# Kernel optimization log

Measured on AMD Instinct MI355X. Metric: run time of the kernel, lower is better.

The kernel has to match this reference:

```python
import jax, jax.numpy as jnp
import numpy as np

# model constants (match init_kwargs)
D_EQUI = 64
D_INV = 256
D_INV_COND = 256
D_MSG = 64
N_HEADS = 16
D_FF = 256
D_EDGE_IN = 64
D_EDGE_OUT = 64
D_OUT = D_EQUI + N_HEADS + D_EDGE_OUT  # 144
IN_FEATS = 2 * D_MSG + D_EQUI + D_EDGE_IN  # 256
NEG = -1e9

B, N, NC = 2, 256, 512


def setup_inputs() -> dict:
    key = jax.random.key(0)
    ks = jax.random.split(key, 20)
    s = 0.02
    inp = {
        'equis': jax.random.normal(ks[0], (B, N, 3, D_EQUI), jnp.float32),
        'invs': jax.random.normal(ks[1], (B, N, D_INV), jnp.float32),
        'cond_equis': jax.random.normal(ks[2], (B, NC, 3, D_EQUI), jnp.float32),
        'cond_invs': jax.random.normal(ks[3], (B, NC, D_INV_COND), jnp.float32),
        'edges': jax.random.normal(ks[4], (B, N, NC, D_EDGE_IN), jnp.float32),
        'adj_matrix': jax.random.randint(ks[5], (B, N, NC), 0, 2, jnp.int32),
        # pairwise message params
        'q_w': s * jax.random.normal(ks[6], (D_INV, D_MSG), jnp.float32),
        'q_b': jnp.zeros((D_MSG,), jnp.float32),
        'k_w': s * jax.random.normal(ks[7], (D_INV_COND, D_MSG), jnp.float32),
        'k_b': jnp.zeros((D_MSG,), jnp.float32),
        'w1': s * jax.random.normal(ks[8], (IN_FEATS, D_FF), jnp.float32),
        'b1': jnp.zeros((D_FF,), jnp.float32),
        'w2': s * jax.random.normal(ks[9], (D_FF, D_OUT), jnp.float32),
        'b2': jnp.zeros((D_OUT,), jnp.float32),
        # equi attention params (bias-free linears)
        'equi_in_w': s * jax.random.normal(ks[10], (D_EQUI, D_EQUI), jnp.float32),
        'equi_out_w': s * jax.random.normal(ks[11], (D_EQUI, D_EQUI), jnp.float32),
        # inv attention params
        'inv_in_w': s * jax.random.normal(ks[12], (D_INV_COND, D_INV_COND), jnp.float32),
        'inv_in_b': jnp.zeros((D_INV_COND,), jnp.float32),
        'inv_out_w': s * jax.random.normal(ks[13], (D_INV_COND, D_INV), jnp.float32),
        'inv_out_b': jnp.zeros((D_INV,), jnp.float32),
    }
    return inp


def reference(equis, invs, cond_equis, cond_invs, edges, adj_matrix,
              q_w, q_b, k_w, k_b, w1, b1, w2, b2,
              equi_in_w, equi_out_w, inv_in_w, inv_in_b, inv_out_w, inv_out_b):
    # adjacency -> additive attention mask [B,N,NC]
    mask = jnp.where(adj_matrix > 0, 0.0, NEG).astype(equis.dtype)

    # ---- pairwise messages ----
    # per-channel dot products over the coordinate axis: [B,N,NC,D_EQUI]
    dot = jnp.einsum('bqxd,bkxd->bqkd', equis, cond_equis)
    q_msg = invs @ q_w + q_b            # [B,N,D_MSG]
    k_msg = cond_invs @ k_w + k_b       # [B,NC,D_MSG]
    feats = jnp.concatenate([
        jnp.broadcast_to(q_msg[:, :, None, :], (B, N, NC, D_MSG)),
        jnp.broadcast_to(k_msg[:, None, :, :], (B, N, NC, D_MSG)),
        dot,
        edges,
    ], axis=-1)                          # [B,N,NC,IN_FEATS]
    h = jax.nn.silu(feats @ w1 + b1)
    messages = h @ w2 + b2               # [B,N,NC,D_OUT]

    equi_m = messages[..., :D_EQUI]
    inv_m = messages[..., D_EQUI:D_EQUI + N_HEADS]
    edge_out = messages[..., D_EQUI + N_HEADS:]

    # ---- equivariant attention ----
    proj = jnp.einsum('bkxd,de->bkxe', cond_equis, equi_in_w)  # [B,NC,3,D_EQUI]
    attn_e = jax.nn.softmax(equi_m + mask[..., None], axis=2)   # [B,N,NC,D_EQUI]
    eo = jnp.einsum('bqkd,bkxd->bqxd', attn_e, proj)            # [B,N,3,D_EQUI]
    w_e = jnp.sqrt(jnp.sum(attn_e ** 2, axis=2))                # [B,N,D_EQUI]
    eo = eo * w_e[:, :, None, :]
    equi_out = jnp.einsum('bqxd,de->bqxe', eo, equi_out_w)

    # ---- invariant attention ----
    pf = cond_invs @ inv_in_w + inv_in_b                        # [B,NC,D_INV_COND]
    hf = pf.reshape(B, NC, N_HEADS, D_INV_COND // N_HEADS)      # [B,NC,H,dh]
    attn_i = jax.nn.softmax(inv_m + mask[..., None], axis=2)    # [B,N,NC,H]
    io = jnp.einsum('bqkh,bkhd->bqhd', attn_i, hf)              # [B,N,H,dh]
    w_i = jnp.sqrt(jnp.sum(attn_i ** 2, axis=2))                # [B,N,H]
    io = (io * w_i[..., None]).reshape(B, N, D_INV_COND)
    inv_out = io @ inv_out_w + inv_out_b                        # [B,N,D_INV]

    return equi_out, inv_out, edge_out
```

## Files before the change

### kernel.cpp

```cpp
#include <hip/hip_runtime.h>
#include <hip/hip_bf16.h>

#define DEVINL static __device__ __forceinline__

typedef __attribute__((ext_vector_type(8))) short bf16x8;
typedef __attribute__((ext_vector_type(8))) unsigned short us8;
typedef __attribute__((ext_vector_type(4))) float f32x4;
typedef __attribute__((ext_vector_type(4))) unsigned short us4;

DEVINL float siluf(float x) { return x / (1.0f + __expf(-x)); }
DEVINL unsigned short bfb(float x) { __hip_bfloat16 h = __float2bfloat16(x); return *(unsigned short*)&h; }
DEVINL float b2f(unsigned short u) { return __uint_as_float(((unsigned int)u) << 16); }

__global__ __launch_bounds__(256) void prep_all(
    const float* __restrict__ invs, const float* __restrict__ cond_invs,
    const float* __restrict__ cond_equis,
    const float* __restrict__ q_w, const float* __restrict__ q_b,
    const float* __restrict__ k_w, const float* __restrict__ k_b,
    const float* __restrict__ w1, const float* __restrict__ b1,
    const float* __restrict__ w2,
    const float* __restrict__ equi_in_w,
    const float* __restrict__ inv_in_w, const float* __restrict__ inv_in_b,
    unsigned short* __restrict__ w1f, unsigned short* __restrict__ w2f,
    float* __restrict__ km, float* __restrict__ hq,
    float* __restrict__ projt, float* __restrict__ pft) {
  __shared__ float smem_f[1024];
  const int blk = blockIdx.x, tid = threadIdx.x;

  if (blk < 25) {
    const int g = blk;
    if (g < 16) {
      #pragma unroll
      for (int e2 = 0; e2 < 16; ++e2) {
        const int flat = tid * 16 + e2;
        const int kk = flat >> 9, rem = flat & 511, ln = rem >> 3, e = rem & 7;
        const int c = g * 16 + (ln & 15);
        const int k = kk * 32 + (ln >> 4) * 8 + e;
        w1f[(size_t)g * 4096 + flat] = bfb(w1[(size_t)k * 256 + c]);
      }
    } else {
      const int t = g - 16;
      #pragma unroll
      for (int e2 = 0; e2 < 16; ++e2) {
        const int flat = tid * 16 + e2;
        const int kk = flat >> 9, rem = flat & 511, ln = rem >> 3, e = rem & 7;
        const int c = t * 16 + (ln & 15);
        const int k = kk * 32 + (ln >> 4) * 8 + e;
        w2f[(size_t)t * 4096 + flat] = bfb(w2[(size_t)k * 144 + c]);
      }
    }
    return;
  }
  if (blk < 281) {
    const int row = (blk - 25) * 4 + (tid >> 6), c = tid & 63;
    float* srow = smem_f + (tid >> 6) * 256;
    for (int k = c; k < 256; k += 64) srow[k] = cond_invs[(size_t)row * 256 + k];
    __syncthreads();
    float a = k_b[c];
    for (int k = 0; k < 256; ++k) a += srow[k] * k_w[(size_t)k * 64 + c];
    km[(size_t)row * 64 + c] = a;
    return;
  }
  if (blk < 1049) {
    const int r = (blk - 281) * 4 + (tid >> 6), c = tid & 63;
    float* srow = smem_f + (tid >> 6) * 64;
    srow[c] = cond_equis[(size_t)r * 64 + c];
    __syncthreads();
    float a = 0.f;
    for (int k = 0; k < 64; ++k) a += srow[k] * equi_in_w[(size_t)k * 64 + c];
    const int b = r / 1536, rr = r % 1536, kn = rr / 3, x = rr % 3;
    projt[((size_t)(b * 3 + x) * 64 + c) * 512 + kn] = a;
    return;
  }
  if (blk < 2073) {
    const int r = blk - 1049, b = r >> 9, kn = r & 511;
    smem_f[tid] = cond_invs[(size_t)r * 256 + tid];
    __syncthreads();
    float a = inv_in_b[tid];
    for (int k = 0; k < 256; ++k) a += smem_f[k] * inv_in_w[(size_t)k * 256 + tid];
    pft[((size_t)(b * 256) + tid) * 512 + kn] = a;
    return;
  }
  {
    const int r = blk - 2073;
    smem_f[tid] = invs[(size_t)r * 256 + tid];
    __syncthreads();
    if (tid < 64) {
      float a = q_b[tid];
      for (int k = 0; k < 256; ++k) a += smem_f[k] * q_w[(size_t)k * 64 + tid];
      smem_f[256 + tid] = a;
    }
    __syncthreads();
    float a = b1[tid];
    for (int d = 0; d < 64; ++d) a += smem_f[256 + d] * w1[(size_t)d * 256 + tid];
    hq[(size_t)r * 256 + tid] = a;
  }
}

__global__ __launch_bounds__(256, 2) void msg_kernel(
    const float* __restrict__ equis, const float* __restrict__ cond_equis,
    const float* __restrict__ edges,
    const float* __restrict__ hq, const float* __restrict__ km,
    const unsigned short* __restrict__ w1f,
    const unsigned short* __restrict__ w2f, const float* __restrict__ b2,
    float* __restrict__ edge_out, __hip_bfloat16* __restrict__ sct) {
  __shared__ __align__(16) unsigned short buf[64][264];
  unsigned short (*score_s)[92] = (unsigned short (*)[92])&buf[0][0];
  float (*edge_s)[68]           = (float (*)[68])((char*)&buf[0][0] + 11776);

  const int bq = blockIdx.x >> 3;
  const int b  = bq >> 8;
  const int k0 = (blockIdx.x & 7) * 64;
  const int tid = threadIdx.x;
  const int lane = tid & 63, wn = tid >> 6;
  const int lj  = lane & 15;
  const int lkb = (lane >> 4) * 8;
  const int lr4 = (lane >> 4) * 4;

  #pragma unroll
  for (int it = 0; it < 4; ++it) {
    const int flat = it * 256 + tid, row = flat >> 4, seg = flat & 15;
    const float4 v = *(const float4*)&km[((size_t)(b * 512 + k0 + row)) * 64 + seg * 4];
    us4 u = { bfb(v.x), bfb(v.y), bfb(v.z), bfb(v.w) };
    *(us4*)&buf[row][seg * 4] = u;
  }
  #pragma unroll
  for (int it = 0; it < 4; ++it) {
    const int flat = it * 256 + tid, row = flat >> 4, seg = flat & 15;
    const float4 v = *(const float4*)&edges[((size_t)bq * 512 + k0 + row) * 64 + seg * 4];
    us4 u = { bfb(v.x), bfb(v.y), bfb(v.z), bfb(v.w) };
    *(us4*)&buf[row][128 + seg * 4] = u;
  }
  {
    const int r = tid >> 2, dseg = tid & 3;
    const float* cer = cond_equis + ((size_t)(b * 512 + k0 + r)) * 192 + dseg * 16;
    const float* eqr = equis + (size_t)bq * 192 + dseg * 16;
    float dv[16];
    #pragma unroll
    for (int j = 0; j < 16; ++j) dv[j] = 0.f;
    #pragma unroll
    for (int sec = 0; sec < 3; ++sec) {
      #pragma unroll
      for (int q4 = 0; q4 < 4; ++q4) {
        const float4 cv = *(const float4*)&cer[sec * 64 + q4 * 4];
        const float4 ev = *(const float4*)&eqr[sec * 64 + q4 * 4];
        dv[q4 * 4 + 0] += cv.x * ev.x;
        dv[q4 * 4 + 1] += cv.y * ev.y;
        dv[q4 * 4 + 2] += cv.z * ev.z;
        dv[q4 * 4 + 3] += cv.w * ev.w;
      }
    }
    us8 o0, o1;
    #pragma unroll
    for (int j = 0; j < 8; ++j) { o0[j] = bfb(dv[j]); o1[j] = bfb(dv[8 + j]); }
    *(us8*)&buf[r][64 + dseg * 16] = o0;
    *(us8*)&buf[r][64 + dseg * 16 + 8] = o1;
  }
  __syncthreads();

#define LW1(BUF, KK) { \
    _Pragma("unroll") for (int ct = 0; ct < 4; ++ct) \
      BUF[ct] = *(const bf16x8*)&w1f[((size_t)(((wn * 4 + ct) * 8 + ((KK) + 2)) * 64) + lane) * 8]; }

#define G1STEP(KK, CUR, NXT, DOPF) { \
    if (DOPF) { LW1(NXT, (KK) + 1); } \
    bf16x8 fbv[4]; \
    _Pragma("unroll") for (int rt = 0; rt < 4; ++rt) \
      fbv[rt] = *(const bf16x8*)&buf[rt * 16 + lj][(KK) * 32 + lkb]; \
    _Pragma("unroll") for (int ct = 0; ct < 4; ++ct) \
      _Pragma("unroll") for (int rt = 0; rt < 4; ++rt) \
        acc[ct][rt] = __builtin_amdgcn_mfma_f32_16x16x32_bf16(CUR[ct], fbv[rt], acc[ct][rt], 0, 0, 0); }

#define LW2(BUF, KK) { \
    _Pragma("unroll") for (int it = 0; it < 3; ++it) { \
      const int t = it * 4 + wn; \
      if (t < 9) BUF[it] = *(const bf16x8*)&w2f[((size_t)((t * 8 + (KK)) * 64) + lane) * 8]; } }

#define G2STEP(KK, CUR, NXT, DOPF) { \
    if (DOPF) { LW2(NXT, (KK) + 1); } \
    bf16x8 fbv[4]; \
    _Pragma("unroll") for (int rt = 0; rt < 4; ++rt) \
      fbv[rt] = *(const bf16x8*)&buf[rt * 16 + lj][(KK) * 32 + lkb]; \
    _Pragma("unroll") for (int it = 0; it < 3; ++it) { \
      const int t = it * 4 + wn; \
      if (t < 9) { \
        _Pragma("unroll") for (int rt = 0; rt < 4; ++rt) \
          a2[it][rt] = __builtin_amdgcn_mfma_f32_16x16x32_bf16(CUR[it], fbv[rt], a2[it][rt], 0, 0, 0); \
      } } }

  f32x4 acc[4][4];
  #pragma unroll
  for (int ct = 0; ct < 4; ++ct) {
    const float4 hv = *(const float4*)&hq[(size_t)bq * 256 + wn * 64 + ct * 16 + lr4];
    #pragma unroll
    for (int rt = 0; rt < 4; ++rt) { acc[ct][rt][0] = hv.x; acc[ct][rt][1] = hv.y; acc[ct][rt][2] = hv.z; acc[ct][rt][3] = hv.w; }
  }
  {
    bf16x8 waA[4], waB[4];
    LW1(waA, 0);
    G1STEP(0, waA, waB, 1)
    G1STEP(1, waB, waA, 1)
    G1STEP(2, waA, waB, 1)
    G1STEP(3, waB, waA, 1)
    G1STEP(4, waA, waB, 1)
    G1STEP(5, waB, waA, 0)
  }
  __syncthreads();

  #pragma unroll
  for (int ct = 0; ct < 4; ++ct)
    #pragma unroll
    for (int rt = 0; rt < 4; ++rt) {
      us4 u = { bfb(siluf(acc[ct][rt][0])), bfb(siluf(acc[ct][rt][1])),
                bfb(siluf(acc[ct][rt][2])), bfb(siluf(acc[ct][rt][3])) };
      *(us4*)&buf[rt * 16 + lj][wn * 64 + ct * 16 + lr4] = u;
    }
  __syncthreads();

  f32x4 a2[3][4];
  #pragma unroll
  for (int it = 0; it < 3; ++it) {
    const int t = it * 4 + wn;
    if (t < 9) {
      const float4 bb = *(const float4*)&b2[t * 16 + lr4];
      #pragma unroll
      for (int rt = 0; rt < 4; ++rt) { a2[it][rt][0] = bb.x; a2[it][rt][1] = bb.y; a2[it][rt][2] = bb.z; a2[it][rt][3] = bb.w; }
    }
  }
  {
    bf16x8 wbA[3], wbB[3];
    LW2(wbA, 0);
    G2STEP(0, wbA, wbB, 1)
    G2STEP(1, wbB, wbA, 1)
    G2STEP(2, wbA, wbB, 1)
    G2STEP(3, wbB, wbA, 1)
    G2STEP(4, wbA, wbB, 1)
    G2STEP(5, wbB, wbA, 1)
    G2STEP(6, wbA, wbB, 1)
    G2STEP(7, wbB, wbA, 0)
  }
  __syncthreads();

  #pragma unroll
  for (int it = 0; it < 3; ++it) {
    const int t = it * 4 + wn;
    if (t < 9) {
      if (t < 5) {
        #pragma unroll
        for (int rt = 0; rt < 4; ++rt) {
          us4 u = { bfb(a2[it][rt][0]), bfb(a2[it][rt][1]), bfb(a2[it][rt][2]), bfb(a2[it][rt][3]) };
          *(us4*)&score_s[rt * 16 + lj][t * 16 + lr4] = u;
        }
      } else {
        #pragma unroll
        for (int rt = 0; rt < 4; ++rt) {
          float4 v; v.x = a2[it][rt][0]; v.y = a2[it][rt][1]; v.z = a2[it][rt][2]; v.w = a2[it][rt][3];
          *(float4*)&edge_s[rt * 16 + lj][(t - 5) * 16 + lr4] = v;
        }
      }
    }
  }
  __syncthreads();

  #pragma unroll
  for (int it = 0; it < 3; ++it) {
    const int idx = it * 256 + tid;
    if (idx < 640) {
      const int c = idx >> 3, s = idx & 7;
      bf16x8 v;
      #pragma unroll
      for (int j = 0; j < 8; ++j) v[j] = (short)score_s[s * 8 + j][c];
      *(bf16x8*)&sct[((size_t)bq * 80 + c) * 512 + k0 + s * 8] = v;
    }
  }
  #pragma unroll
  for (int it = 0; it < 4; ++it) {
    const int idx = it * 256 + tid;
    const int row = idx >> 4, sg = idx & 15;
    *(float4*)&edge_out[((size_t)bq * 512 + k0 + row) * 64 + sg * 4] = *(const float4*)&edge_s[row][sg * 4];
  }
#undef LW1
#undef G1STEP
#undef LW2
#undef G2STEP
}

__global__ __launch_bounds__(512) void attn_kernel(
    const __hip_bfloat16* __restrict__ sct, const int* __restrict__ adj,
    const float* __restrict__ projt, const float* __restrict__ pft,
    const float* __restrict__ eow, const float* __restrict__ iow,
    const float* __restrict__ iob, float* __restrict__ out) {
  __shared__ float eo_s[3][64];
  __shared__ float io_s[256];
  __shared__ __align__(16) float wred[8][64][20];

  const int bq = blockIdx.x, b = bq >> 8;
  const int tid = threadIdx.x, lane = tid & 63, w = tid >> 6;
  const int kb = lane * 8;

  const int4 aj0 = *(const int4*)&adj[(size_t)bq * 512 + kb];
  const int4 aj1 = *(const int4*)&adj[(size_t)bq * 512 + kb + 4];
  const unsigned int mk = (aj0.x > 0 ? 1u : 0) | (aj0.y > 0 ? 2u : 0) | (aj0.z > 0 ? 4u : 0) | (aj0.w > 0 ? 8u : 0)
                        | (aj1.x > 0 ? 16u : 0) | (aj1.y > 0 ? 32u : 0) | (aj1.z > 0 ? 64u : 0) | (aj1.w > 0 ? 128u : 0);

  for (int dd = 0; dd < 8; ++dd) {
    const int d = w * 8 + dd;
    const bf16x8 s8 = *(const bf16x8*)&sct[((size_t)bq * 80 + d) * 512 + kb];
    float p[8], z = 0.f, s2 = 0.f;
    #pragma unroll
    for (int j = 0; j < 8; ++j) {
      const float e = ((mk >> j) & 1) ? __expf(b2f((unsigned short)s8[j])) : 0.f;
      p[j] = e; z += e; s2 += e * e;
    }
    float ax[3];
    #pragma unroll
    for (int x = 0; x < 3; ++x) {
      const float* pr = projt + ((size_t)(b * 3 + x) * 64 + d) * 512 + kb;
      const float4 w0 = *(const float4*)pr;
      const float4 w1v = *(const float4*)(pr + 4);
      ax[x] = p[0] * w0.x + p[1] * w0.y + p[2] * w0.z + p[3] * w0.w
            + p[4] * w1v.x + p[5] * w1v.y + p[6] * w1v.z + p[7] * w1v.w;
    }
    #pragma unroll
    for (int off = 32; off; off >>= 1) {
      z += __shfl_xor(z, off, 64); s2 += __shfl_xor(s2, off, 64);
      ax[0] += __shfl_xor(ax[0], off, 64); ax[1] += __shfl_xor(ax[1], off, 64); ax[2] += __shfl_xor(ax[2], off, 64);
    }
    if (lane == 0) {
      const float sc = sqrtf(s2) / (z * z);
      eo_s[0][d] = ax[0] * sc; eo_s[1][d] = ax[1] * sc; eo_s[2][d] = ax[2] * sc;
    }
  }

  #pragma unroll
  for (int hh = 0; hh < 2; ++hh) {
    const int h = w * 2 + hh;
    const bf16x8 s8 = *(const bf16x8*)&sct[((size_t)bq * 80 + 64 + h) * 512 + kb];
    float p[8], z = 0.f, s2 = 0.f;
    #pragma unroll
    for (int j = 0; j < 8; ++j) {
      const float e = ((mk >> j) & 1) ? __expf(b2f((unsigned short)s8[j])) : 0.f;
      p[j] = e; z += e; s2 += e * e;
    }
    f32x4 io[4];
    #pragma unroll
    for (int d4 = 0; d4 < 4; ++d4)
      #pragma unroll
      for (int di = 0; di < 4; ++di) {
        const float* pr = pft + ((size_t)(b * 256) + h * 16 + d4 * 4 + di) * 512 + kb;
        const float4 w0 = *(const float4*)pr;
        const float4 w1v = *(const float4*)(pr + 4);
        io[d4][di] = p[0] * w0.x + p[1] * w0.y + p[2] * w0.z + p[3] * w0.w
                   + p[4] * w1v.x + p[5] * w1v.y + p[6] * w1v.z + p[7] * w1v.w;
      }
    #pragma unroll
    for (int off = 32; off; off >>= 1) { z += __shfl_xor(z, off, 64); s2 += __shfl_xor(s2, off, 64); }
    #pragma unroll
    for (int d4 = 0; d4 < 4; ++d4) {
      float4 vv; vv.x = io[d4][0]; vv.y = io[d4][1]; vv.z = io[d4][2]; vv.w = io[d4][3];
      *(float4*)&wred[w][lane][d4 * 4] = vv;
    }
    const int g = lane >> 4, dd2 = lane & 15;
    float s = 0.f;
    #pragma unroll
    for (int j = 0; j < 16; ++j) s += wred[w][g * 16 + j][dd2];
    s += __shfl_xor(s, 16, 64);
    s += __shfl_xor(s, 32, 64);
    if (lane < 16) {
      const float sc = sqrtf(s2) / (z * z);
      io_s[h * 16 + dd2] = s * sc;
    }
  }
  __syncthreads();

  if (tid < 192) {
    const int x = tid >> 6, e = tid & 63;
    float a = 0.f;
    for (int d = 0; d < 64; ++d) a += eo_s[x][d] * eow[(size_t)d * 64 + e];
    out[(size_t)bq * 192 + x * 64 + e] = a;
  }
  if (tid < 256) {
    float a = iob[tid];
    for (int k = 0; k < 256; ++k) a += io_s[k] * iow[(size_t)k * 256 + tid];
    out[98304 + (size_t)bq * 256 + tid] = a;
  }
}

extern "C" void kernel_launch(void* const* d_in, const int* in_sizes, int n_in,
                              void* d_out, int out_size, void* d_ws, size_t ws_size,
                              hipStream_t stream) {
  const float* equis      = (const float*)d_in[0];
  const float* invs       = (const float*)d_in[1];
  const float* cond_equis = (const float*)d_in[2];
  const float* cond_invs  = (const float*)d_in[3];
  const float* edges      = (const float*)d_in[4];
  const int*   adj        = (const int*)d_in[5];
  const float* q_w  = (const float*)d_in[6];
  const float* q_b  = (const float*)d_in[7];
  const float* k_w  = (const float*)d_in[8];
  const float* k_b  = (const float*)d_in[9];
  const float* w1   = (const float*)d_in[10];
  const float* b1   = (const float*)d_in[11];
  const float* w2   = (const float*)d_in[12];
  const float* b2   = (const float*)d_in[13];
  const float* equi_in_w  = (const float*)d_in[14];
  const float* equi_out_w = (const float*)d_in[15];
  const float* inv_in_w   = (const float*)d_in[16];
  const float* inv_in_b   = (const float*)d_in[17];
  const float* inv_out_w  = (const float*)d_in[18];
  const float* inv_out_b  = (const float*)d_in[19];

  float* out = (float*)d_out;
  float* ws  = (float*)d_ws;
  unsigned short* w1f = (unsigned short*)ws;
  unsigned short* w2f = w1f + 65536;
  float* km    = ws + 51200;
  float* hq    = km + 65536;
  float* projt = hq + 131072;
  float* pft   = projt + 196608;
  __hip_bfloat16* sct = (__hip_bfloat16*)(pft + 262144);

  prep_all<<<2585, 256, 0, stream>>>(invs, cond_invs, cond_equis,
                                     q_w, q_b, k_w, k_b, w1, b1, w2,
                                     equi_in_w, inv_in_w, inv_in_b,
                                     w1f, w2f, km, hq, projt, pft);

  msg_kernel<<<4096, 256, 0, stream>>>(equis, cond_equis, edges, hq, km,
                                       w1f, w2f, b2,
                                       out + 229376 , sct);

  attn_kernel<<<512, 512, 0, stream>>>(sct, adj, projt, pft,
                                       equi_out_w, inv_out_w, inv_out_b, out);
}
```

Baseline: 156.5 us.

## Make msg_kernel persistent over four key tiles with software-prefetched inputs

Each msg_kernel block now handles four consecutive 64-key tiles (half of the keys for one query) instead of one, cutting the grid from 4096 to 1024 blocks. The next tile's km, edges and cond_equis values are loaded into registers before the first GEMM and written to a separate feats shared buffer during the hidden-activation phase, so global loads overlap MFMA work. Query equis are cached once in shared memory. The costs are more registers (prefetch buffers plus accumulators), more shared memory (a feats buffer in addition to hbuf), and fewer blocks, which may lower occupancy and load balance across CUs.

After: 397.8 us. +154.3%, slower.

```diff
diff --git a/kernel.cpp b/kernel.cpp
--- a/kernel.cpp
+++ b/kernel.cpp
@@ -104,59 +104,66 @@
     const unsigned short* __restrict__ w1f,
     const unsigned short* __restrict__ w2f, const float* __restrict__ b2,
     float* __restrict__ edge_out, __hip_bfloat16* __restrict__ sct) {
-  __shared__ __align__(16) unsigned short buf[64][264];
-  unsigned short (*score_s)[92] = (unsigned short (*)[92])&buf[0][0];
-  float (*edge_s)[68]           = (float (*)[68])((char*)&buf[0][0] + 11776);
-
-  const int bq = blockIdx.x >> 3;
+  __shared__ __align__(16) unsigned short feats[64][200];
+  __shared__ __align__(16) unsigned short hbuf[64][264];
+  __shared__ float eq_s[192];
+  unsigned short (*score_s)[92] = (unsigned short (*)[92])&hbuf[0][0];
+  float (*edge_s)[68]           = (float (*)[68])((char*)&hbuf[0][0] + 11776);
+
+  const int bq = blockIdx.x >> 1;
   const int b  = bq >> 8;
-  const int k0 = (blockIdx.x & 7) * 64;
+  const int kh = blockIdx.x & 1;
   const int tid = threadIdx.x;
   const int lane = tid & 63, wn = tid >> 6;
   const int lj  = lane & 15;
   const int lkb = (lane >> 4) * 8;
   const int lr4 = (lane >> 4) * 4;
 
-  #pragma unroll
-  for (int it = 0; it < 4; ++it) {
-    const int flat = it * 256 + tid, row = flat >> 4, seg = flat & 15;
-    const float4 v = *(const float4*)&km[((size_t)(b * 512 + k0 + row)) * 64 + seg * 4];
-    us4 u = { bfb(v.x), bfb(v.y), bfb(v.z), bfb(v.w) };
-    *(us4*)&buf[row][seg * 4] = u;
-  }
-  #pragma unroll
-  for (int it = 0; it < 4; ++it) {
-    const int flat = it * 256 + tid, row = flat >> 4, seg = flat & 15;
-    const float4 v = *(const float4*)&edges[((size_t)bq * 512 + k0 + row) * 64 + seg * 4];
-    us4 u = { bfb(v.x), bfb(v.y), bfb(v.z), bfb(v.w) };
-    *(us4*)&buf[row][128 + seg * 4] = u;
-  }
+  if (tid < 192) eq_s[tid] = equis[(size_t)bq * 192 + tid];
+
   {
-    const int r = tid >> 2, dseg = tid & 3;
-    const float* cer = cond_equis + ((size_t)(b * 512 + k0 + r)) * 192 + dseg * 16;
-    const float* eqr = equis + (size_t)bq * 192 + dseg * 16;
-    float dv[16];
-    #pragma unroll
-    for (int j = 0; j < 16; ++j) dv[j] = 0.f;
-    #pragma unroll
-    for (int sec = 0; sec < 3; ++sec) {
-      #pragma unroll
-      for (int q4 = 0; q4 < 4; ++q4) {
-        const float4 cv = *(const float4*)&cer[sec * 64 + q4 * 4];
-        const float4 ev = *(const float4*)&eqr[sec * 64 + q4 * 4];
-        dv[q4 * 4 + 0] += cv.x * ev.x;
-        dv[q4 * 4 + 1] += cv.y * ev.y;
-        dv[q4 * 4 + 2] += cv.z * ev.z;
-        dv[q4 * 4 + 3] += cv.w * ev.w;
-      }
-    }
-    us8 o0, o1;
-    #pragma unroll
-    for (int j = 0; j < 8; ++j) { o0[j] = bfb(dv[j]); o1[j] = bfb(dv[8 + j]); }
-    *(us8*)&buf[r][64 + dseg * 16] = o0;
-    *(us8*)&buf[r][64 + dseg * 16 + 8] = o1;
-  }
-  __syncthreads();
+    const int k0 = kh * 256;
+    #pragma unroll
+    for (int it = 0; it < 4; ++it) {
+      const int flat = it * 256 + tid, row = flat >> 4, seg = flat & 15;
+      const float4 v = *(const float4*)&km[((size_t)(b * 512 + k0 + row)) * 64 + seg * 4];
+      us4 u = { bfb(v.x), bfb(v.y), bfb(v.z), bfb(v.w) };
+      *(us4*)&feats[row][seg * 4] = u;
+    }
+    #pragma unroll
+    for (int it = 0; it < 4; ++it) {
+      const int flat = it * 256 + tid, row = flat >> 4, seg = flat & 15;
+      const float4 v = *(const float4*)&edges[((size_t)bq * 512 + k0 + row) * 64 + seg * 4];
+      us4 u = { bfb(v.x), bfb(v.y), bfb(v.z), bfb(v.w) };
+      *(us4*)&feats[row][128 + seg * 4] = u;
+    }
+    __syncthreads();
+    {
+      const int r = tid >> 2, dseg = tid & 3;
+      const float* cer = cond_equis + ((size_t)(b * 512 + k0 + r)) * 192 + dseg * 16;
+      float dv[16];
+      #pragma unroll
+      for (int j = 0; j < 16; ++j) dv[j] = 0.f;
+      #pragma unroll
+      for (int sec = 0; sec < 3; ++sec) {
+        #pragma unroll
+        for (int q4 = 0; q4 < 4; ++q4) {
+          const float4 cv = *(const float4*)&cer[sec * 64 + q4 * 4];
+          const float4 ev = *(const float4*)&eq_s[sec * 64 + dseg * 16 + q4 * 4];
+          dv[q4 * 4 + 0] += cv.x * ev.x;
+          dv[q4 * 4 + 1] += cv.y * ev.y;
+          dv[q4 * 4 + 2] += cv.z * ev.z;
+          dv[q4 * 4 + 3] += cv.w * ev.w;
+        }
+      }
+      us8 o0, o1;
+      #pragma unroll
+      for (int j = 0; j < 8; ++j) { o0[j] = bfb(dv[j]); o1[j] = bfb(dv[8 + j]); }
+      *(us8*)&feats[r][64 + dseg * 16] = o0;
+      *(us8*)&feats[r][64 + dseg * 16 + 8] = o1;
+    }
+    __syncthreads();
+  }
 
 #define LW1(BUF, KK) { \
     _Pragma("unroll") for (int ct = 0; ct < 4; ++ct) \
@@ -166,7 +173,7 @@
     if (DOPF) { LW1(NXT, (KK) + 1); } \
     bf16x8 fbv[4]; \
     _Pragma("unroll") for (int rt = 0; rt < 4; ++rt) \
-      fbv[rt] = *(const bf16x8*)&buf[rt * 16 + lj][(KK) * 32 + lkb]; \
+      fbv[rt] = *(const bf16x8*)&feats[rt * 16 + lj][(KK) * 32 + lkb]; \
     _Pragma("unroll") for (int ct = 0; ct < 4; ++ct) \
       _Pragma("unroll") for (int rt = 0; rt < 4; ++rt) \
         acc[ct][rt] = __builtin_amdgcn_mfma_f32_16x16x32_bf16(CUR[ct], fbv[rt], acc[ct][rt], 0, 0, 0); }
@@ -180,7 +187,7 @@
     if (DOPF) { LW2(NXT, (KK) + 1); } \
     bf16x8 fbv[4]; \
     _Pragma("unroll") for (int rt = 0; rt < 4; ++rt) \
-      fbv[rt] = *(const bf16x8*)&buf[rt * 16 + lj][(KK) * 32 + lkb]; \
+      fbv[rt] = *(const bf16x8*)&hbuf[rt * 16 + lj][(KK) * 32 + lkb]; \
     _Pragma("unroll") for (int it = 0; it < 3; ++it) { \
       const int t = it * 4 + wn; \
       if (t < 9) { \
@@ -188,96 +195,150 @@
           a2[it][rt] = __builtin_amdgcn_mfma_f32_16x16x32_bf16(CUR[it], fbv[rt], a2[it][rt], 0, 0, 0); \
       } } }
 
-  f32x4 acc[4][4];
-  #pragma unroll
-  for (int ct = 0; ct < 4; ++ct) {
-    const float4 hv = *(const float4*)&hq[(size_t)bq * 256 + wn * 64 + ct * 16 + lr4];
-    #pragma unroll
-    for (int rt = 0; rt < 4; ++rt) { acc[ct][rt][0] = hv.x; acc[ct][rt][1] = hv.y; acc[ct][rt][2] = hv.z; acc[ct][rt][3] = hv.w; }
-  }
-  {
-    bf16x8 waA[4], waB[4];
-    LW1(waA, 0);
-    G1STEP(0, waA, waB, 1)
-    G1STEP(1, waB, waA, 1)
-    G1STEP(2, waA, waB, 1)
-    G1STEP(3, waB, waA, 1)
-    G1STEP(4, waA, waB, 1)
-    G1STEP(5, waB, waA, 0)
-  }
-  __syncthreads();
-
-  #pragma unroll
-  for (int ct = 0; ct < 4; ++ct)
-    #pragma unroll
-    for (int rt = 0; rt < 4; ++rt) {
-      us4 u = { bfb(siluf(acc[ct][rt][0])), bfb(siluf(acc[ct][rt][1])),
-                bfb(siluf(acc[ct][rt][2])), bfb(siluf(acc[ct][rt][3])) };
-      *(us4*)&buf[rt * 16 + lj][wn * 64 + ct * 16 + lr4] = u;
-    }
-  __syncthreads();
-
-  f32x4 a2[3][4];
-  #pragma unroll
-  for (int it = 0; it < 3; ++it) {
-    const int t = it * 4 + wn;
-    if (t < 9) {
-      const float4 bb = *(const float4*)&b2[t * 16 + lr4];
-      #pragma unroll
-      for (int rt = 0; rt < 4; ++rt) { a2[it][rt][0] = bb.x; a2[it][rt][1] = bb.y; a2[it][rt][2] = bb.z; a2[it][rt][3] = bb.w; }
-    }
-  }
-  {
-    bf16x8 wbA[3], wbB[3];
-    LW2(wbA, 0);
-    G2STEP(0, wbA, wbB, 1)
-    G2STEP(1, wbB, wbA, 1)
-    G2STEP(2, wbA, wbB, 1)
-    G2STEP(3, wbB, wbA, 1)
-    G2STEP(4, wbA, wbB, 1)
-    G2STEP(5, wbB, wbA, 1)
-    G2STEP(6, wbA, wbB, 1)
-    G2STEP(7, wbB, wbA, 0)
-  }
-  __syncthreads();
-
-  #pragma unroll
-  for (int it = 0; it < 3; ++it) {
-    const int t = it * 4 + wn;
-    if (t < 9) {
-      if (t < 5) {
+  for (int t = 0; t < 4; ++t) {
+    const int k0  = kh * 256 + t * 64;
+    const int k0n = k0 + 64;
+    const bool pf = (t < 3);
+
+    float4 pkm[4], ped[4], pc[3][4];
+    if (pf) {
+      #pragma unroll
+      for (int it = 0; it < 4; ++it) {
+        const int flat = it * 256 + tid, row = flat >> 4, seg = flat & 15;
+        pkm[it] = *(const float4*)&km[((size_t)(b * 512 + k0n + row)) * 64 + seg * 4];
+        ped[it] = *(const float4*)&edges[((size_t)bq * 512 + k0n + row) * 64 + seg * 4];
+      }
+      const int r = tid >> 2, dseg = tid & 3;
+      const float* cer = cond_equis + ((size_t)(b * 512 + k0n + r)) * 192 + dseg * 16;
+      #pragma unroll
+      for (int sec = 0; sec < 3; ++sec)
         #pragma unroll
-        for (int rt = 0; rt < 4; ++rt) {
-          us4 u = { bfb(a2[it][rt][0]), bfb(a2[it][rt][1]), bfb(a2[it][rt][2]), bfb(a2[it][rt][3]) };
-          *(us4*)&score_s[rt * 16 + lj][t * 16 + lr4] = u;
+        for (int q4 = 0; q4 < 4; ++q4)
+          pc[sec][q4] = *(const float4*)&cer[sec * 64 + q4 * 4];
+    }
+
+    f32x4 acc[4][4];
+    #pragma unroll
+    for (int ct = 0; ct < 4; ++ct) {
+      const float4 hv = *(const float4*)&hq[(size_t)bq * 256 + wn * 64 + ct * 16 + lr4];
+      #pragma unroll
+      for (int rt = 0; rt < 4; ++rt) { acc[ct][rt][0] = hv.x; acc[ct][rt][1] = hv.y; acc[ct][rt][2] = hv.z; acc[ct][rt][3] = hv.w; }
+    }
+    {
+      bf16x8 waA[4], waB[4];
+      LW1(waA, 0);
+      G1STEP(0, waA, waB, 1)
+      G1STEP(1, waB, waA, 1)
+      G1STEP(2, waA, waB, 1)
+      G1STEP(3, waB, waA, 1)
+      G1STEP(4, waA, waB, 1)
+      G1STEP(5, waB, waA, 0)
+    }
+    __syncthreads();
+
+    #pragma unroll
+    for (int ct = 0; ct < 4; ++ct)
+      #pragma unroll
+      for (int rt = 0; rt < 4; ++rt) {
+        us4 u = { bfb(siluf(acc[ct][rt][0])), bfb(siluf(acc[ct][rt][1])),
+                  bfb(siluf(acc[ct][rt][2])), bfb(siluf(acc[ct][rt][3])) };
+        *(us4*)&hbuf[rt * 16 + lj][wn * 64 + ct * 16 + lr4] = u;
+      }
+    if (pf) {
+      #pragma unroll
+      for (int it = 0; it < 4; ++it) {
+        const int flat = it * 256 + tid, row = flat >> 4, seg = flat & 15;
+        us4 uk = { bfb(pkm[it].x), bfb(pkm[it].y), bfb(pkm[it].z), bfb(pkm[it].w) };
+        *(us4*)&feats[row][seg * 4] = uk;
+        us4 ue = { bfb(ped[it].x), bfb(ped[it].y), bfb(ped[it].z), bfb(ped[it].w) };
+        *(us4*)&feats[row][128 + seg * 4] = ue;
+      }
+      const int r = tid >> 2, dseg = tid & 3;
+      float dv[16];
+      #pragma unroll
+      for (int j = 0; j < 16; ++j) dv[j] = 0.f;
+      #pragma unroll
+      for (int sec = 0; sec < 3; ++sec) {
+        #pragma unroll
+        for (int q4 = 0; q4 < 4; ++q4) {
+          const float4 cv = pc[sec][q4];
+          const float4 ev = *(const float4*)&eq_s[sec * 64 + dseg * 16 + q4 * 4];
+          dv[q4 * 4 + 0] += cv.x * ev.x;
+          dv[q4 * 4 + 1] += cv.y * ev.y;
+          dv[q4 * 4 + 2] += cv.z * ev.z;
+          dv[q4 * 4 + 3] += cv.w * ev.w;
         }
-      } else {
+      }
+      us8 o0, o1;
+      #pragma unroll
+      for (int j = 0; j < 8; ++j) { o0[j] = bfb(dv[j]); o1[j] = bfb(dv[8 + j]); }
+      *(us8*)&feats[r][64 + dseg * 16] = o0;
+      *(us8*)&feats[r][64 + dseg * 16 + 8] = o1;
+    }
+    __syncthreads();
+
+    f32x4 a2[3][4];
+    #pragma unroll
+    for (int it = 0; it < 3; ++it) {
+      const int t2 = it * 4 + wn;
+      if (t2 < 9) {
+        const float4 bb = *(const float4*)&b2[t2 * 16 + lr4];
         #pragma unroll
-        for (int rt = 0; rt < 4; ++rt) {
-          float4 v; v.x = a2[it][rt][0]; v.y = a2[it][rt][1]; v.z = a2[it][rt][2]; v.w = a2[it][rt][3];
-          *(float4*)&edge_s[rt * 16 + lj][(t - 5) * 16 + lr4] = v;
+        for (int rt = 0; rt < 4; ++rt) { a2[it][rt][0] = bb.x; a2[it][rt][1] = bb.y; a2[it][rt][2] = bb.z; a2[it][rt][3] = bb.w; }
+      }
+    }
+    {
+      bf16x8 wbA[3], wbB[3];
+      LW2(wbA, 0);
+      G2STEP(0, wbA, wbB, 1)
+      G2STEP(1, wbB, wbA, 1)
+      G2STEP(2, wbA, wbB, 1)
+      G2STEP(3, wbB, wbA, 1)
+      G2STEP(4, wbA, wbB, 1)
+      G2STEP(5, wbB, wbA, 1)
+      G2STEP(6, wbA, wbB, 1)
+      G2STEP(7, wbB, wbA, 0)
+    }
+    __syncthreads();
+
+    #pragma unroll
+    for (int it = 0; it < 3; ++it) {
+      const int t2 = it * 4 + wn;
+      if (t2 < 9) {
+        if (t2 < 5) {
+          #pragma unroll
+          for (int rt = 0; rt < 4; ++rt) {
+            us4 u = { bfb(a2[it][rt][0]), bfb(a2[it][rt][1]), bfb(a2[it][rt][2]), bfb(a2[it][rt][3]) };
+            *(us4*)&score_s[rt * 16 + lj][t2 * 16 + lr4] = u;
+          }
+        } else {
+          #pragma unroll
+          for (int rt = 0; rt < 4; ++rt) {
+            float4 v; v.x = a2[it][rt][0]; v.y = a2[it][rt][1]; v.z = a2[it][rt][2]; v.w = a2[it][rt][3];
+            *(float4*)&edge_s[rt * 16 + lj][(t2 - 5) * 16 + lr4] = v;
+          }
         }
       }
     }
-  }
-  __syncthreads();
-
-  #pragma unroll
-  for (int it = 0; it < 3; ++it) {
-    const int idx = it * 256 + tid;
-    if (idx < 640) {
-      const int c = idx >> 3, s = idx & 7;
-      bf16x8 v;
-      #pragma unroll
-      for (int j = 0; j < 8; ++j) v[j] = (short)score_s[s * 8 + j][c];
-      *(bf16x8*)&sct[((size_t)bq * 80 + c) * 512 + k0 + s * 8] = v;
-    }
-  }
-  #pragma unroll
-  for (int it = 0; it < 4; ++it) {
-    const int idx = it * 256 + tid;
-    const int row = idx >> 4, sg = idx & 15;
-    *(float4*)&edge_out[((size_t)bq * 512 + k0 + row) * 64 + sg * 4] = *(const float4*)&edge_s[row][sg * 4];
+    __syncthreads();
+
+    #pragma unroll
+    for (int it = 0; it < 3; ++it) {
+      const int idx = it * 256 + tid;
+      if (idx < 640) {
+        const int c = idx >> 3, s = idx & 7;
+        bf16x8 v;
+        #pragma unroll
+        for (int j = 0; j < 8; ++j) v[j] = (short)score_s[s * 8 + j][c];
+        *(bf16x8*)&sct[((size_t)bq * 80 + c) * 512 + k0 + s * 8] = v;
+      }
+    }
+    #pragma unroll
+    for (int it = 0; it < 4; ++it) {
+      const int idx = it * 256 + tid;
+      const int row = idx >> 4, sg = idx & 15;
+      *(float4*)&edge_out[((size_t)bq * 512 + k0 + row) * 64 + sg * 4] = *(const float4*)&edge_s[row][sg * 4];
+    }
   }
 #undef LW1
 #undef G1STEP
@@ -425,7 +486,7 @@
                                      equi_in_w, inv_in_w, inv_in_b,
                                      w1f, w2f, km, hq, projt, pft);
 
-  msg_kernel<<<4096, 256, 0, stream>>>(equis, cond_equis, edges, hq, km,
+  msg_kernel<<<1024, 256, 0, stream>>>(equis, cond_equis, edges, hq, km,
                                        w1f, w2f, b2,
                                        out + 229376 , sct);
 
```

## Make msg_kernel persistent per query row with register-resident W1 fragments

Applied to the files above, without the earlier changes.

Each msg_kernel block now handles one query row and loops over all 8 key tiles of 64, instead of launching one block per tile. The first-layer W1 fragments are loaded into registers once per block and reused across tiles, which removes repeated global weight loads. The attention kernel's block index is also permuted, which changes the order in which query rows are scheduled. In exchange the grid shrinks from 4096 to 512 blocks, so fewer blocks are available to hide latency, and 24 extra bf16x8 registers per thread may lower occupancy.

Result: slower. 285.7 us (+82.6%).

```diff
diff --git a/kernel.cpp b/kernel.cpp
--- a/kernel.cpp
+++ b/kernel.cpp
@@ -108,68 +108,28 @@
   unsigned short (*score_s)[92] = (unsigned short (*)[92])&buf[0][0];
   float (*edge_s)[68]           = (float (*)[68])((char*)&buf[0][0] + 11776);
 
-  const int bq = blockIdx.x >> 3;
+  const int bq = blockIdx.x;
   const int b  = bq >> 8;
-  const int k0 = (blockIdx.x & 7) * 64;
   const int tid = threadIdx.x;
   const int lane = tid & 63, wn = tid >> 6;
   const int lj  = lane & 15;
   const int lkb = (lane >> 4) * 8;
   const int lr4 = (lane >> 4) * 4;
 
+  bf16x8 w1r[4][6];
   #pragma unroll
-  for (int it = 0; it < 4; ++it) {
-    const int flat = it * 256 + tid, row = flat >> 4, seg = flat & 15;
-    const float4 v = *(const float4*)&km[((size_t)(b * 512 + k0 + row)) * 64 + seg * 4];
-    us4 u = { bfb(v.x), bfb(v.y), bfb(v.z), bfb(v.w) };
-    *(us4*)&buf[row][seg * 4] = u;
-  }
-  #pragma unroll
-  for (int it = 0; it < 4; ++it) {
-    const int flat = it * 256 + tid, row = flat >> 4, seg = flat & 15;
-    const float4 v = *(const float4*)&edges[((size_t)bq * 512 + k0 + row) * 64 + seg * 4];
-    us4 u = { bfb(v.x), bfb(v.y), bfb(v.z), bfb(v.w) };
-    *(us4*)&buf[row][128 + seg * 4] = u;
-  }
-  {
-    const int r = tid >> 2, dseg = tid & 3;
-    const float* cer = cond_equis + ((size_t)(b * 512 + k0 + r)) * 192 + dseg * 16;
-    const float* eqr = equis + (size_t)bq * 192 + dseg * 16;
-    float dv[16];
-    #pragma unroll
-    for (int j = 0; j < 16; ++j) dv[j] = 0.f;
-    #pragma unroll
-    for (int sec = 0; sec < 3; ++sec) {
-      #pragma unroll
-      for (int q4 = 0; q4 < 4; ++q4) {
-        const float4 cv = *(const float4*)&cer[sec * 64 + q4 * 4];
-        const float4 ev = *(const float4*)&eqr[sec * 64 + q4 * 4];
-        dv[q4 * 4 + 0] += cv.x * ev.x;
-        dv[q4 * 4 + 1] += cv.y * ev.y;
-        dv[q4 * 4 + 2] += cv.z * ev.z;
-        dv[q4 * 4 + 3] += cv.w * ev.w;
-      }
-    }
-    us8 o0, o1;
-    #pragma unroll
-    for (int j = 0; j < 8; ++j) { o0[j] = bfb(dv[j]); o1[j] = bfb(dv[8 + j]); }
-    *(us8*)&buf[r][64 + dseg * 16] = o0;
-    *(us8*)&buf[r][64 + dseg * 16 + 8] = o1;
-  }
-  __syncthreads();
-
-#define LW1(BUF, KK) { \
-    _Pragma("unroll") for (int ct = 0; ct < 4; ++ct) \
-      BUF[ct] = *(const bf16x8*)&w1f[((size_t)(((wn * 4 + ct) * 8 + ((KK) + 2)) * 64) + lane) * 8]; }
-
-#define G1STEP(KK, CUR, NXT, DOPF) { \
-    if (DOPF) { LW1(NXT, (KK) + 1); } \
+  for (int ct = 0; ct < 4; ++ct)
+    #pragma unroll
+    for (int kk = 0; kk < 6; ++kk)
+      w1r[ct][kk] = *(const bf16x8*)&w1f[((size_t)(((wn * 4 + ct) * 8 + (kk + 2)) * 64) + lane) * 8];
+
+#define G1STEP(KK) { \
     bf16x8 fbv[4]; \
     _Pragma("unroll") for (int rt = 0; rt < 4; ++rt) \
       fbv[rt] = *(const bf16x8*)&buf[rt * 16 + lj][(KK) * 32 + lkb]; \
     _Pragma("unroll") for (int ct = 0; ct < 4; ++ct) \
       _Pragma("unroll") for (int rt = 0; rt < 4; ++rt) \
-        acc[ct][rt] = __builtin_amdgcn_mfma_f32_16x16x32_bf16(CUR[ct], fbv[rt], acc[ct][rt], 0, 0, 0); }
+        acc[ct][rt] = __builtin_amdgcn_mfma_f32_16x16x32_bf16(w1r[ct][KK], fbv[rt], acc[ct][rt], 0, 0, 0); }
 
 #define LW2(BUF, KK) { \
     _Pragma("unroll") for (int it = 0; it < 3; ++it) { \
@@ -188,98 +148,134 @@
           a2[it][rt] = __builtin_amdgcn_mfma_f32_16x16x32_bf16(CUR[it], fbv[rt], a2[it][rt], 0, 0, 0); \
       } } }
 
-  f32x4 acc[4][4];
-  #pragma unroll
-  for (int ct = 0; ct < 4; ++ct) {
-    const float4 hv = *(const float4*)&hq[(size_t)bq * 256 + wn * 64 + ct * 16 + lr4];
-    #pragma unroll
-    for (int rt = 0; rt < 4; ++rt) { acc[ct][rt][0] = hv.x; acc[ct][rt][1] = hv.y; acc[ct][rt][2] = hv.z; acc[ct][rt][3] = hv.w; }
-  }
-  {
-    bf16x8 waA[4], waB[4];
-    LW1(waA, 0);
-    G1STEP(0, waA, waB, 1)
-    G1STEP(1, waB, waA, 1)
-    G1STEP(2, waA, waB, 1)
-    G1STEP(3, waB, waA, 1)
-    G1STEP(4, waA, waB, 1)
-    G1STEP(5, waB, waA, 0)
-  }
-  __syncthreads();
-
-  #pragma unroll
-  for (int ct = 0; ct < 4; ++ct)
-    #pragma unroll
-    for (int rt = 0; rt < 4; ++rt) {
-      us4 u = { bfb(siluf(acc[ct][rt][0])), bfb(siluf(acc[ct][rt][1])),
-                bfb(siluf(acc[ct][rt][2])), bfb(siluf(acc[ct][rt][3])) };
-      *(us4*)&buf[rt * 16 + lj][wn * 64 + ct * 16 + lr4] = u;
-    }
-  __syncthreads();
-
-  f32x4 a2[3][4];
-  #pragma unroll
-  for (int it = 0; it < 3; ++it) {
-    const int t = it * 4 + wn;
-    if (t < 9) {
-      const float4 bb = *(const float4*)&b2[t * 16 + lr4];
-      #pragma unroll
-      for (int rt = 0; rt < 4; ++rt) { a2[it][rt][0] = bb.x; a2[it][rt][1] = bb.y; a2[it][rt][2] = bb.z; a2[it][rt][3] = bb.w; }
-    }
-  }
-  {
-    bf16x8 wbA[3], wbB[3];
-    LW2(wbA, 0);
-    G2STEP(0, wbA, wbB, 1)
-    G2STEP(1, wbB, wbA, 1)
-    G2STEP(2, wbA, wbB, 1)
-    G2STEP(3, wbB, wbA, 1)
-    G2STEP(4, wbA, wbB, 1)
-    G2STEP(5, wbB, wbA, 1)
-    G2STEP(6, wbA, wbB, 1)
-    G2STEP(7, wbB, wbA, 0)
-  }
-  __syncthreads();
-
-  #pragma unroll
-  for (int it = 0; it < 3; ++it) {
-    const int t = it * 4 + wn;
-    if (t < 9) {
-      if (t < 5) {
+  for (int t8 = 0; t8 < 8; ++t8) {
+    const int k0 = t8 * 64;
+
+    #pragma unroll
+    for (int it = 0; it < 4; ++it) {
+      const int flat = it * 256 + tid, row = flat >> 4, seg = flat & 15;
+      const float4 v = *(const float4*)&km[((size_t)(b * 512 + k0 + row)) * 64 + seg * 4];
+      us4 u = { bfb(v.x), bfb(v.y), bfb(v.z), bfb(v.w) };
+      *(us4*)&buf[row][seg * 4] = u;
+    }
+    #pragma unroll
+    for (int it = 0; it < 4; ++it) {
+      const int flat = it * 256 + tid, row = flat >> 4, seg = flat & 15;
+      const float4 v = *(const float4*)&edges[((size_t)bq * 512 + k0 + row) * 64 + seg * 4];
+      us4 u = { bfb(v.x), bfb(v.y), bfb(v.z), bfb(v.w) };
+      *(us4*)&buf[row][128 + seg * 4] = u;
+    }
+    {
+      const int r = tid >> 2, dseg = tid & 3;
+      const float* cer = cond_equis + ((size_t)(b * 512 + k0 + r)) * 192 + dseg * 16;
+      const float* eqr = equis + (size_t)bq * 192 + dseg * 16;
+      float dv[16];
+      #pragma unroll
+      for (int j = 0; j < 16; ++j) dv[j] = 0.f;
+      #pragma unroll
+      for (int sec = 0; sec < 3; ++sec) {
         #pragma unroll
-        for (int rt = 0; rt < 4; ++rt) {
-          us4 u = { bfb(a2[it][rt][0]), bfb(a2[it][rt][1]), bfb(a2[it][rt][2]), bfb(a2[it][rt][3]) };
-          *(us4*)&score_s[rt * 16 + lj][t * 16 + lr4] = u;
+        for (int q4 = 0; q4 < 4; ++q4) {
+          const float4 cv = *(const float4*)&cer[sec * 64 + q4 * 4];
+          const float4 ev = *(const float4*)&eqr[sec * 64 + q4 * 4];
+          dv[q4 * 4 + 0] += cv.x * ev.x;
+          dv[q4 * 4 + 1] += cv.y * ev.y;
+          dv[q4 * 4 + 2] += cv.z * ev.z;
+          dv[q4 * 4 + 3] += cv.w * ev.w;
         }
-      } else {
+      }
+      us8 o0, o1;
+      #pragma unroll
+      for (int j = 0; j < 8; ++j) { o0[j] = bfb(dv[j]); o1[j] = bfb(dv[8 + j]); }
+      *(us8*)&buf[r][64 + dseg * 16] = o0;
+      *(us8*)&buf[r][64 + dseg * 16 + 8] = o1;
+    }
+    __syncthreads();
+
+    f32x4 acc[4][4];
+    #pragma unroll
+    for (int ct = 0; ct < 4; ++ct) {
+      const float4 hv = *(const float4*)&hq[(size_t)bq * 256 + wn * 64 + ct * 16 + lr4];
+      #pragma unroll
+      for (int rt = 0; rt < 4; ++rt) { acc[ct][rt][0] = hv.x; acc[ct][rt][1] = hv.y; acc[ct][rt][2] = hv.z; acc[ct][rt][3] = hv.w; }
+    }
+    G1STEP(0) G1STEP(1) G1STEP(2) G1STEP(3) G1STEP(4) G1STEP(5)
+    __syncthreads();
+
+    #pragma unroll
+    for (int ct = 0; ct < 4; ++ct)
+      #pragma unroll
+      for (int rt = 0; rt < 4; ++rt) {
+        us4 u = { bfb(siluf(acc[ct][rt][0])), bfb(siluf(acc[ct][rt][1])),
+                  bfb(siluf(acc[ct][rt][2])), bfb(siluf(acc[ct][rt][3])) };
+        *(us4*)&buf[rt * 16 + lj][wn * 64 + ct * 16 + lr4] = u;
+      }
+    __syncthreads();
+
+    f32x4 a2[3][4];
+    #pragma unroll
+    for (int it = 0; it < 3; ++it) {
+      const int t = it * 4 + wn;
+      if (t < 9) {
+        const float4 bb = *(const float4*)&b2[t * 16 + lr4];
         #pragma unroll
-        for (int rt = 0; rt < 4; ++rt) {
-          float4 v; v.x = a2[it][rt][0]; v.y = a2[it][rt][1]; v.z = a2[it][rt][2]; v.w = a2[it][rt][3];
-          *(float4*)&edge_s[rt * 16 + lj][(t - 5) * 16 + lr4] = v;
+        for (int rt = 0; rt < 4; ++rt) { a2[it][rt][0] = bb.x; a2[it][rt][1] = bb.y; a2[it][rt][2] = bb.z; a2[it][rt][3] = bb.w; }
+      }
+    }
+    {
+      bf16x8 wbA[3], wbB[3];
+      LW2(wbA, 0);
+      G2STEP(0, wbA, wbB, 1)
+      G2STEP(1, wbB, wbA, 1)
+      G2STEP(2, wbA, wbB, 1)
+      G2STEP(3, wbB, wbA, 1)
+      G2STEP(4, wbA, wbB, 1)
+      G2STEP(5, wbB, wbA, 1)
+      G2STEP(6, wbA, wbB, 1)
+      G2STEP(7, wbB, wbA, 0)
+    }
+    __syncthreads();
+
+    #pragma unroll
+    for (int it = 0; it < 3; ++it) {
+      const int t2 = it * 4 + wn;
+      if (t2 < 9) {
+        if (t2 < 5) {
+          #pragma unroll
+          for (int rt = 0; rt < 4; ++rt) {
+            us4 u = { bfb(a2[it][rt][0]), bfb(a2[it][rt][1]), bfb(a2[it][rt][2]), bfb(a2[it][rt][3]) };
+            *(us4*)&score_s[rt * 16 + lj][t2 * 16 + lr4] = u;
+          }
+        } else {
+          #pragma unroll
+          for (int rt = 0; rt < 4; ++rt) {
+            float4 v; v.x = a2[it][rt][0]; v.y = a2[it][rt][1]; v.z = a2[it][rt][2]; v.w = a2[it][rt][3];
+            *(float4*)&edge_s[rt * 16 + lj][(t2 - 5) * 16 + lr4] = v;
+          }
         }
       }
     }
-  }
-  __syncthreads();
-
-  #pragma unroll
-  for (int it = 0; it < 3; ++it) {
-    const int idx = it * 256 + tid;
-    if (idx < 640) {
-      const int c = idx >> 3, s = idx & 7;
-      bf16x8 v;
-      #pragma unroll
-      for (int j = 0; j < 8; ++j) v[j] = (short)score_s[s * 8 + j][c];
-      *(bf16x8*)&sct[((size_t)bq * 80 + c) * 512 + k0 + s * 8] = v;
-    }
-  }
-  #pragma unroll
-  for (int it = 0; it < 4; ++it) {
-    const int idx = it * 256 + tid;
-    const int row = idx >> 4, sg = idx & 15;
-    *(float4*)&edge_out[((size_t)bq * 512 + k0 + row) * 64 + sg * 4] = *(const float4*)&edge_s[row][sg * 4];
-  }
-#undef LW1
+    __syncthreads();
+
+    #pragma unroll
+    for (int it = 0; it < 3; ++it) {
+      const int idx = it * 256 + tid;
+      if (idx < 640) {
+        const int c = idx >> 3, s = idx & 7;
+        bf16x8 v;
+        #pragma unroll
+        for (int j = 0; j < 8; ++j) v[j] = (short)score_s[s * 8 + j][c];
+        *(bf16x8*)&sct[((size_t)bq * 80 + c) * 512 + k0 + s * 8] = v;
+      }
+    }
+    #pragma unroll
+    for (int it = 0; it < 4; ++it) {
+      const int idx = it * 256 + tid;
+      const int row = idx >> 4, sg = idx & 15;
+      *(float4*)&edge_out[((size_t)bq * 512 + k0 + row) * 64 + sg * 4] = *(const float4*)&edge_s[row][sg * 4];
+    }
+    __syncthreads();
+  }
 #undef G1STEP
 #undef LW2
 #undef G2STEP
@@ -294,7 +290,8 @@
   __shared__ float io_s[256];
   __shared__ __align__(16) float wred[8][64][20];
 
-  const int bq = blockIdx.x, b = bq >> 8;
+  const int bq = ((blockIdx.x & 7) << 6) + (blockIdx.x >> 3);
+  const int b = bq >> 8;
   const int tid = threadIdx.x, lane = tid & 63, w = tid >> 6;
   const int kb = lane * 8;
 
@@ -425,9 +422,9 @@
                                      equi_in_w, inv_in_w, inv_in_b,
                                      w1f, w2f, km, hq, projt, pft);
 
-  msg_kernel<<<4096, 256, 0, stream>>>(equis, cond_equis, edges, hq, km,
-                                       w1f, w2f, b2,
-                                       out + 229376 , sct);
+  msg_kernel<<<512, 256, 0, stream>>>(equis, cond_equis, edges, hq, km,
+                                      w1f, w2f, b2,
+                                      out + 229376 , sct);
 
   attn_kernel<<<512, 512, 0, stream>>>(sct, adj, projt, pft,
                                        equi_out_w, inv_out_w, inv_out_b, out);
```
